# Optimization experiments

Measured on AMD Instinct MI355X. Metric: run time of the kernel, lower is better.

Reference implementation:

```python
import jax, jax.numpy as jnp
import numpy as np

B, A, N, D_IN, HID, H = 128, 64, 2000, 128, 512, 8
HD = HID // H  # head_dim = 64
ND = 16        # depot agents


def setup_inputs() -> dict:
    key = jax.random.key(0)
    ks = jax.random.split(key, 8)
    s = 0.05  # keep logits well-conditioned
    return {
        "state_t": jax.random.normal(ks[0], (B, A, D_IN), dtype=jnp.float32),
        "context": jax.random.normal(ks[1], (B, N, D_IN), dtype=jnp.float32),
        "context_d": jax.random.normal(ks[2], (B, N, D_IN), dtype=jnp.float32),
        "w_q": jax.random.normal(ks[3], (HID, D_IN), dtype=jnp.float32) * s,
        "w_k1": jax.random.normal(ks[4], (HID, D_IN), dtype=jnp.float32) * s,
        "w_v1": jax.random.normal(ks[5], (HID, D_IN), dtype=jnp.float32) * s,
        "w_fc": jax.random.normal(ks[6], (HID, HID), dtype=jnp.float32) * s,
        "w_k2": jax.random.normal(ks[7], (HID, D_IN), dtype=jnp.float32) * s,
        "n_d": ND,
        "mask": jax.random.randint(jax.random.fold_in(key, 1), (B, A, N), 0, 2, dtype=jnp.int32),
        "T": 1,
    }


def reference(state_t, context, context_d, w_q, w_k1, w_v1, w_fc, w_k2, n_d, mask, T):
    hidden = w_q.shape[0]
    hd = hidden // H
    norm1 = np.float32(1.0 / np.sqrt(hd))
    norm2 = np.float32(1.0 / np.sqrt(hidden))

    def attn1(st, ctx, m):
        b, a, _ = st.shape
        n = ctx.shape[1]
        Q = (st @ w_q.T).reshape(b, a, H, hd).transpose(0, 2, 1, 3)   # (b,H,a,hd)
        K = (ctx @ w_k1.T).reshape(b, n, H, hd).transpose(0, 2, 1, 3)  # (b,H,n,hd)
        V = (ctx @ w_v1.T).reshape(b, n, H, hd).transpose(0, 2, 1, 3)
        comp = norm1 * jnp.einsum('bhad,bhnd->bhan', Q, K)
        u = jnp.where(m[:, None, :, :] != 0, jnp.float32(-10000.0), comp)
        s = jax.nn.softmax(u, axis=-1)
        out = jnp.einsum('bhan,bhnd->bhad', s, V)
        # FAITHFUL to torch: .view(b, a, hidden) on (b,H,a,hd) WITHOUT head transpose
        return out.reshape(b, a, hidden) @ w_fc.T

    x_d = attn1(state_t[:, :n_d], context_d, mask[:, :n_d])       # (B, n_d, HID)
    x_r = attn1(state_t[:, n_d:], context, mask[:, n_d:])         # (B, A-n_d, HID)

    Kd = context_d @ w_k2.T  # (B, N, HID)
    Kr = context @ w_k2.T
    compd = norm2 * jnp.einsum('bad,bnd->ban', x_d, Kd)
    compr = norm2 * jnp.einsum('bad,bnd->ban', x_r, Kr)
    comp = jnp.concatenate([compd, compr], axis=1)                # (B, A, N)
    comp = jnp.where(mask != 0, jnp.float32(-10000.0), comp)
    return jax.nn.softmax(comp / T, axis=-1)
```

## Files before the change

### kernel.cpp

```cpp
#include <hip/hip_runtime.h>

typedef short s16x8 __attribute__((ext_vector_type(8)));
typedef float f32x4 __attribute__((ext_vector_type(4)));

#define B_   128
#define A_   64
#define N_   2000
#define DIN  128
#define HID  512
#define H_   8
#define HD_  64
#define ND_  16
#define NT_  32

__device__ __forceinline__ unsigned short f2bf(float f) {
  union { float f; unsigned int u; } v; v.f = f;
  unsigned int u = v.u;
  unsigned int r = (u + 0x7fffu + ((u >> 16) & 1u)) >> 16;
  return (unsigned short)r;
}

__device__ __forceinline__ float bf2f(unsigned int u16v) {
  union { unsigned int u; float f; } v; v.u = u16v << 16;
  return v.f;
}

__device__ __forceinline__ f32x4 mfma16(s16x8 a, s16x8 b, f32x4 c) {
  return __builtin_amdgcn_mfma_f32_16x16x32_bf16(a, b, c, 0, 0, 0);
}

__device__ __forceinline__ unsigned int cvtpk(float lo, float hi) {
  unsigned int r;
  asm("v_cvt_pk_bf16_f32 %0, %1, %2" : "=v"(r) : "v"(lo), "v"(hi));
  return r;
}

__device__ __forceinline__ void gload16(const void* g, void* l) {
  __builtin_amdgcn_global_load_lds(
      (const __attribute__((address_space(1))) unsigned int*)g,
      (__attribute__((address_space(3))) unsigned int*)l, 16, 0, 0);
}

__device__ __forceinline__ void barrier_lds() {
  asm volatile("s_waitcnt lgkmcnt(0)" ::: "memory");
  __builtin_amdgcn_s_barrier();
  __builtin_amdgcn_sched_barrier(0);
}
__device__ __forceinline__ void barrier_full() {
  asm volatile("s_waitcnt vmcnt(0) lgkmcnt(0)" ::: "memory");
  __builtin_amdgcn_s_barrier();
  __builtin_amdgcn_sched_barrier(0);
}

__global__ __launch_bounds__(256) void k_cvt(const float* __restrict__ src,
                                             unsigned short* __restrict__ dst, int n4) {
  int i = blockIdx.x * blockDim.x + threadIdx.x;
  int stride = gridDim.x * blockDim.x;
  for (; i < n4; i += stride) {
    float4 v = ((const float4*)src)[i];
    ushort4 o;
    o.x = f2bf(v.x); o.y = f2bf(v.y); o.z = f2bf(v.z); o.w = f2bf(v.w);
    ((ushort4*)dst)[i] = o;
  }
}

__global__ __launch_bounds__(256) void k_cvt_t(const float* __restrict__ src,
                                               unsigned short* __restrict__ dst) {
  int i = blockIdx.x * 256 + threadIdx.x;
  int o = i >> 7, d = i & 127;
  dst[d * 512 + o] = f2bf(src[i]);
}

__global__ __launch_bounds__(256) void k_mask(const int* __restrict__ src,
                                              unsigned char* __restrict__ dst, int n4) {
  int i = blockIdx.x * blockDim.x + threadIdx.x;
  int stride = gridDim.x * blockDim.x;
  for (; i < n4; i += stride) {
    int4 v = ((const int4*)src)[i];
    uchar4 o;
    o.x = v.x ? 1 : 0; o.y = v.y ? 1 : 0; o.z = v.z ? 1 : 0; o.w = v.w ? 1 : 0;
    ((uchar4*)dst)[i] = o;
  }
}

template <int BR>
__device__ __forceinline__ void attn_body(
    int sub,
    const unsigned short* __restrict__ st, const unsigned short* __restrict__ C,
    const unsigned short* __restrict__ wq, const unsigned short* __restrict__ wk1,
    const unsigned short* __restrict__ wv1, const unsigned char* __restrict__ mask,
    float* __restrict__ x,
    unsigned short (*ctx_lds)[128], unsigned short (*K_lds)[72],
    unsigned short (*VT_lds)[72], unsigned short (*QP_lds)[72], float (*red_l)[48]) {
  constexpr int AT = BR ? 3 : 1;
  constexpr int a0 = BR ? ND_ : 0;
  const int tid = threadIdx.x;
  const int w = tid >> 6, lane = tid & 63, rn = lane & 15, kq = lane >> 4;
  const int b = sub >> 3, h = sub & 7;
  const int srow = lane >> 4;
  const int scol = lane & 15;

#pragma unroll
  for (int i = 0; i < 4; ++i) {
    int r0 = i * 16 + w * 4;
    int row = r0 + srow;
    const char* g = (const char*)C + (((size_t)b * N_ + row) << 8) + ((scol ^ (row & 7)) << 4);
    gload16(g, (char*)&ctx_lds[0][0] + (r0 << 8));
  }

  s16x8 kfrag[4], vfrag[4];
  {
    const size_t orow = (size_t)(h * HD_ + w * 16 + rn) * DIN;
#pragma unroll
    for (int k = 0; k < 4; ++k) {
      kfrag[k] = *(const s16x8*)(wk1 + orow + k * 32 + kq * 8);
      vfrag[k] = *(const s16x8*)(wv1 + orow + k * 32 + kq * 8);
    }
  }

  {
    s16x8 qw[4];
    const size_t orow = (size_t)(h * HD_ + w * 16 + rn) * DIN;
#pragma unroll
    for (int k = 0; k < 4; ++k) qw[k] = *(const s16x8*)(wq + orow + k * 32 + kq * 8);
#pragma unroll
    for (int at = 0; at < AT; ++at) {
      f32x4 acc = {0.f, 0.f, 0.f, 0.f};
#pragma unroll
      for (int k = 0; k < 4; ++k) {
        s16x8 sf = *(const s16x8*)(st + (size_t)(b * A_ + a0 + at * 16 + rn) * DIN + k * 32 + kq * 8);
        acc = mfma16(qw[k], sf, acc);
      }
      uint2 pk; pk.x = cvtpk(acc[0], acc[1]); pk.y = cvtpk(acc[2], acc[3]);
      *(uint2*)&QP_lds[at * 16 + rn][w * 16 + kq * 4] = pk;
    }
  }
  barrier_lds();

  s16x8 qf[AT][2];
#pragma unroll
  for (int at = 0; at < AT; ++at)
#pragma unroll
    for (int kd = 0; kd < 2; ++kd)
      qf[at][kd] = *(const s16x8*)&QP_lds[at * 16 + rn][kd * 32 + kq * 8];

  f32x4 O[AT];
  float lpart[AT];
#pragma unroll
  for (int at = 0; at < AT; ++at) { O[at] = {0.f, 0.f, 0.f, 0.f}; lpart[at] = 0.f; }

  for (int nt = 0; nt < NT_; ++nt) {
    const int n0 = nt * 64;
    barrier_full();

    unsigned int m4[AT];
    const int ngbase = n0 + w * 16 + kq * 4;
    const int ngc = ngbase > (N_ - 4) ? (N_ - 4) : ngbase;
#pragma unroll
    for (int at = 0; at < AT; ++at)
      m4[at] = *(const unsigned int*)(mask + (size_t)(b * A_ + a0 + at * 16 + rn) * N_ + ngc);

#pragma unroll
    for (int ns = 0; ns < 4; ++ns) {
      s16x8 cf[4];
#pragma unroll
      for (int kd = 0; kd < 4; ++kd)
        cf[kd] = *(const s16x8*)&ctx_lds[ns * 16 + rn][(((kd << 2) | kq) ^ (rn & 7)) << 3];
      f32x4 aK = {0.f, 0.f, 0.f, 0.f}, aV = {0.f, 0.f, 0.f, 0.f};
#pragma unroll
      for (int kd = 0; kd < 4; ++kd) {
        aK = mfma16(kfrag[kd], cf[kd], aK);
        aV = mfma16(cf[kd], vfrag[kd], aV);
      }
      if (n0 + 64 > N_) {
#pragma unroll
        for (int r = 0; r < 4; ++r)
          if (n0 + ns * 16 + kq * 4 + r >= N_) aV[r] = 0.f;
      }
      uint2 pkK; pkK.x = cvtpk(aK[0], aK[1]); pkK.y = cvtpk(aK[2], aK[3]);
      *(uint2*)&K_lds[ns * 16 + rn][w * 16 + kq * 4] = pkK;
      uint2 pkV; pkV.x = cvtpk(aV[0], aV[1]); pkV.y = cvtpk(aV[2], aV[3]);
      *(uint2*)&VT_lds[w * 16 + rn][ns * 16 + kq * 4] = pkV;
    }
    barrier_lds();

    if (nt + 1 < NT_) {
      const int n1 = n0 + 64;
#pragma unroll
      for (int i = 0; i < 4; ++i) {
        int r0 = i * 16 + w * 4;
        int row = r0 + srow;
        const char* g = (const char*)C + (((size_t)b * N_ + n1 + row) << 8) + ((scol ^ (row & 7)) << 4);
        gload16(g, (char*)&ctx_lds[0][0] + (r0 << 8));
      }
    }

    s16x8 kf[2];
#pragma unroll
    for (int kd = 0; kd < 2; ++kd)
      kf[kd] = *(const s16x8*)&K_lds[w * 16 + rn][kd * 32 + kq * 8];
#pragma unroll
    for (int at = 0; at < AT; ++at) {
      f32x4 acc = {0.f, 0.f, 0.f, 0.f};
#pragma unroll
      for (int kd = 0; kd < 2; ++kd) acc = mfma16(kf[kd], qf[at][kd], acc);
      float p[4];
#pragma unroll
      for (int r = 0; r < 4; ++r) {
        bool valid = (ngbase + r < N_) && (((m4[at] >> (8 * r)) & 255u) == 0u);
        float e = valid ? acc[r] * 0.125f - 8.0f : -1.0e4f;
        p[r] = __expf(e);
      }
      lpart[at] += (p[0] + p[1]) + (p[2] + p[3]);
      uint2 pkP; pkP.x = cvtpk(p[0], p[1]); pkP.y = cvtpk(p[2], p[3]);
      *(uint2*)&QP_lds[at * 16 + rn][w * 16 + kq * 4] = pkP;
    }
    barrier_lds();

    s16x8 vtf[2];
#pragma unroll
    for (int kn = 0; kn < 2; ++kn)
      vtf[kn] = *(const s16x8*)&VT_lds[w * 16 + rn][kn * 32 + kq * 8];
#pragma unroll
    for (int at = 0; at < AT; ++at) {
      f32x4 acc = O[at];
#pragma unroll
      for (int kn = 0; kn < 2; ++kn)
        acc = mfma16(*(const s16x8*)&QP_lds[at * 16 + rn][kn * 32 + kq * 8], vtf[kn], acc);
      O[at] = acc;
    }
  }

#pragma unroll
  for (int at = 0; at < AT; ++at) {
    float lp = lpart[at];
    lp += __shfl_xor(lp, 16);
    lp += __shfl_xor(lp, 32);
    if (kq == 0) red_l[w][at * 16 + rn] = lp;
  }
  barrier_lds();
#pragma unroll
  for (int at = 0; at < AT; ++at) {
#pragma unroll
    for (int r = 0; r < 4; ++r) {
      int a = at * 16 + kq * 4 + r;
      float ls = (red_l[0][a] + red_l[1][a]) + (red_l[2][a] + red_l[3][a]);
      float val = O[at][r] / ls;
      int row = BR ? (ND_ + h * 6 + (a >> 3)) : (h * 2 + (a >> 3));
      int col = (a & 7) * HD_ + w * 16 + rn;
      x[((size_t)b * A_ + row) * HID + col] = val;
    }
  }
}

__global__ __launch_bounds__(256) void k_attn1(const unsigned short* __restrict__ st,
                                               const unsigned short* __restrict__ ctx,
                                               const unsigned short* __restrict__ ctxd,
                                               const unsigned short* __restrict__ wq,
                                               const unsigned short* __restrict__ wk1,
                                               const unsigned short* __restrict__ wv1,
                                               const unsigned char* __restrict__ mask,
                                               float* __restrict__ x) {
  __shared__ unsigned short ctx_lds[64][128];
  __shared__ unsigned short K_lds[64][72];
  __shared__ unsigned short VT_lds[64][72];
  __shared__ unsigned short QP_lds[48][72];
  __shared__ float red_l[4][48];
  const int bid = blockIdx.x;
  const int sub = bid >> 1;
  if (bid & 1)
    attn_body<1>(sub, st, ctx, wq, wk1, wv1, mask, x, ctx_lds, K_lds, VT_lds, QP_lds, red_l);
  else
    attn_body<0>(sub, st, ctxd, wq, wk1, wv1, mask, x, ctx_lds, K_lds, VT_lds, QP_lds, red_l);
}

__global__ __launch_bounds__(256) void k_fc2(const float* __restrict__ x,
                                             const unsigned short* __restrict__ wfc,
                                             const unsigned short* __restrict__ wk2t,
                                             unsigned short* __restrict__ y2b) {
  __shared__ unsigned short x2_lds[16][520];
  const int tid = threadIdx.x;
  const int w = tid >> 6;
  const int lane = tid & 63;
  const int rn = lane & 15, kq = lane >> 4;
  const size_t rowbase = (size_t)blockIdx.x * 16;
  const float norm2 = 0.04419417382415922f;

  f32x4 acc[8];
#pragma unroll
  for (int ot = 0; ot < 8; ++ot) acc[ot] = {0.f, 0.f, 0.f, 0.f};

  for (int k = 0; k < 16; ++k) {
    const float* ap = x + (rowbase + rn) * HID + k * 32 + kq * 8;
    float4 a1 = *(const float4*)ap;
    float4 a2 = *(const float4*)(ap + 4);
    s16x8 af;
    af[0] = (short)f2bf(a1.x); af[1] = (short)f2bf(a1.y);
    af[2] = (short)f2bf(a1.z); af[3] = (short)f2bf(a1.w);
    af[4] = (short)f2bf(a2.x); af[5] = (short)f2bf(a2.y);
    af[6] = (short)f2bf(a2.z); af[7] = (short)f2bf(a2.w);
#pragma unroll
    for (int ot = 0; ot < 8; ++ot) {
      s16x8 bf = *(const s16x8*)(wfc + (size_t)(w * 128 + ot * 16 + rn) * HID + k * 32 + kq * 8);
      acc[ot] = mfma16(af, bf, acc[ot]);
    }
  }
#pragma unroll
  for (int ot = 0; ot < 8; ++ot)
#pragma unroll
    for (int r = 0; r < 4; ++r)
      x2_lds[kq * 4 + r][w * 128 + ot * 16 + rn] = f2bf(acc[ot][r]);
  __syncthreads();

#pragma unroll
  for (int j = 0; j < 2; ++j) {
    const int d0 = w * 32 + j * 16;
    f32x4 acc2 = {0.f, 0.f, 0.f, 0.f};
    for (int kk = 0; kk < 16; ++kk) {
      s16x8 af2 = *(const s16x8*)&x2_lds[rn][kk * 32 + kq * 8];
      s16x8 bf2 = *(const s16x8*)(wk2t + (size_t)(d0 + rn) * HID + kk * 32 + kq * 8);
      acc2 = mfma16(af2, bf2, acc2);
    }
#pragma unroll
    for (int r = 0; r < 4; ++r)
      y2b[(rowbase + kq * 4 + r) * DIN + d0 + rn] = f2bf(acc2[r] * norm2);
  }
}

__global__ __launch_bounds__(256) void k_logits_sm(const unsigned short* __restrict__ ctx,
                                                   const unsigned short* __restrict__ ctxd,
                                                   const unsigned short* __restrict__ y2b,
                                                   const unsigned char* __restrict__ mask,
                                                   const int* __restrict__ Tptr,
                                                   float* __restrict__ out) {
  __shared__ unsigned short ctx_lds[3][64][128];
  __shared__ unsigned short p_lds[16][2048];
  __shared__ float red_l[4][16];

  const int tid = threadIdx.x;
  const int w = tid >> 6, lane = tid & 63, rn = lane & 15, kq = lane >> 4;
  const int atile = blockIdx.x;
  const int b = blockIdx.y;
  const int a0 = atile * 16;
  const unsigned short* __restrict__ C = atile ? ctx : ctxd;
  const float Tinv = 1.0f / (float)Tptr[0];
  const int srow = lane >> 4, scol = lane & 15;
  const size_t bN = (size_t)b * N_;
  const size_t mrow = (size_t)(b * A_ + a0 + rn) * N_;

  s16x8 yf[4];
#pragma unroll
  for (int kd = 0; kd < 4; ++kd)
    yf[kd] = *(const s16x8*)(y2b + (size_t)(b * A_ + a0 + rn) * DIN + kd * 32 + kq * 8);

  unsigned int mcur = *(const unsigned int*)(mask + mrow + w * 16 + kq * 4);
#pragma unroll
  for (int i = 0; i < 4; ++i) {
    int r0 = i * 16 + w * 4;
    int row = r0 + srow;
    gload16((const char*)C + ((bN + row) << 8) + ((scol ^ (row & 7)) << 4),
            (char*)&ctx_lds[0][0][0] + (r0 << 8));
  }
#pragma unroll
  for (int i = 0; i < 4; ++i) {
    int r0 = i * 16 + w * 4;
    int row = r0 + srow;
    gload16((const char*)C + ((bN + 64 + row) << 8) + ((scol ^ (row & 7)) << 4),
            (char*)&ctx_lds[1][0][0] + (r0 << 8));
  }

  float lpart = 0.f;
  for (int nt = 0; nt < NT_; ++nt) {
    const int n0 = nt * 64;
    if (nt == 0) { asm volatile("s_waitcnt vmcnt(4)" ::: "memory"); }
    else         { asm volatile("s_waitcnt vmcnt(5)" ::: "memory"); }
    __builtin_amdgcn_s_barrier();
    __builtin_amdgcn_sched_barrier(0);

    unsigned int mnext;
    {
      int nb1 = (nt + 1 < NT_ ? nt + 1 : 0) * 64 + w * 16 + kq * 4;
      int ngc = nb1 > (N_ - 4) ? (N_ - 4) : nb1;
      mnext = *(const unsigned int*)(mask + mrow + ngc);
    }
    {
      int t2 = nt + 2 < NT_ ? nt + 2 : 0;
      char* dstb = (char*)&ctx_lds[(nt + 2) % 3][0][0];
#pragma unroll
      for (int i = 0; i < 4; ++i) {
        int r0 = i * 16 + w * 4;
        int row = r0 + srow;
        gload16((const char*)C + ((bN + t2 * 64 + row) << 8) + ((scol ^ (row & 7)) << 4),
                dstb + (r0 << 8));
      }
    }

    const unsigned short (*buf)[128] = ctx_lds[nt % 3];
    f32x4 acc = {0.f, 0.f, 0.f, 0.f};
#pragma unroll
    for (int kd = 0; kd < 4; ++kd) {
      s16x8 cf = *(const s16x8*)&buf[w * 16 + rn][(((kd << 2) | kq) ^ (rn & 7)) << 3];
      acc = mfma16(cf, yf[kd], acc);
    }
    const int nbase = n0 + w * 16 + kq * 4;
    float pv[4];
#pragma unroll
    for (int r = 0; r < 4; ++r) {
      bool valid = (nbase + r < N_) && (((mcur >> (8 * r)) & 255u) == 0u);
      pv[r] = valid ? __expf(acc[r] * Tinv - 8.0f) : 0.f;
    }
    lpart += (pv[0] + pv[1]) + (pv[2] + pv[3]);
    uint2 pk; pk.x = cvtpk(pv[0], pv[1]); pk.y = cvtpk(pv[2], pv[3]);
    int bo = (rn << 12) + (nbase << 1);
    *(uint2*)((char*)p_lds + (bo ^ ((rn & 7) << 4))) = pk;
    mcur = mnext;
  }

  float lp = lpart;
  lp += __shfl_xor(lp, 16);
  lp += __shfl_xor(lp, 32);
  if (kq == 0) red_l[w][rn] = lp;
  barrier_full();

  const size_t outbase = ((size_t)b * A_ + a0) * (size_t)N_;
  for (int row = 0; row < 16; ++row) {
    float l = (red_l[0][row] + red_l[1][row]) + (red_l[2][row] + red_l[3][row]);
    float inv = 1.0f / l;
    if (tid < 250) {
      const char* srcp = (const char*)p_lds + (row << 12) + ((tid ^ (row & 7)) << 4);
      uint2 pk = *(const uint2*)srcp;
      float4 o0, o1;
      o0.x = bf2f(pk.x & 0xFFFFu) * inv;
      o0.y = bf2f(pk.x >> 16) * inv;
      o0.z = bf2f(pk.y & 0xFFFFu) * inv;
      o0.w = bf2f(pk.y >> 16) * inv;
      const char* srcp2 = srcp + 8;
      uint2 pk2 = *(const uint2*)srcp2;
      o1.x = bf2f(pk2.x & 0xFFFFu) * inv;
      o1.y = bf2f(pk2.x >> 16) * inv;
      o1.z = bf2f(pk2.y & 0xFFFFu) * inv;
      o1.w = bf2f(pk2.y >> 16) * inv;
      float* op = out + outbase + (size_t)row * N_ + tid * 8;
      *(float4*)op = o0;
      *(float4*)(op + 4) = o1;
    }
  }
}

extern "C" void kernel_launch(void* const* d_in, const int* in_sizes, int n_in,
                              void* d_out, int out_size, void* d_ws, size_t ws_size,
                              hipStream_t stream) {
  const float* state_t   = (const float*)d_in[0];
  const float* context   = (const float*)d_in[1];
  const float* context_d = (const float*)d_in[2];
  const float* w_q  = (const float*)d_in[3];
  const float* w_k1 = (const float*)d_in[4];
  const float* w_v1 = (const float*)d_in[5];
  const float* w_fc = (const float*)d_in[6];
  const float* w_k2 = (const float*)d_in[7];
  const int* maski  = (const int*)d_in[9];
  const int* Tptr   = (const int*)d_in[10];
  float* out = (float*)d_out;

  char* ws = (char*)d_ws;
  unsigned short* ctxb  = (unsigned short*)ws; ws += (size_t)B_ * N_ * DIN * 2;
  unsigned short* ctxdb = (unsigned short*)ws; ws += (size_t)B_ * N_ * DIN * 2;
  unsigned short* stb   = (unsigned short*)ws; ws += (size_t)B_ * A_ * DIN * 2;
  unsigned short* wqb   = (unsigned short*)ws; ws += (size_t)HID * DIN * 2;
  unsigned short* wk1b  = (unsigned short*)ws; ws += (size_t)HID * DIN * 2;
  unsigned short* wv1b  = (unsigned short*)ws; ws += (size_t)HID * DIN * 2;
  unsigned short* wk2t  = (unsigned short*)ws; ws += (size_t)HID * DIN * 2;
  unsigned short* wfcb  = (unsigned short*)ws; ws += (size_t)HID * HID * 2;
  unsigned char*  mask8 = (unsigned char*)ws;  ws += (size_t)B_ * A_ * N_;
  float*          x     = (float*)ws;          ws += (size_t)B_ * A_ * HID * 4;
  unsigned short* y2b   = (unsigned short*)ws; ws += (size_t)B_ * A_ * DIN * 2;

  k_cvt<<<2048, 256, 0, stream>>>(context,   ctxb,  B_ * N_ * DIN / 4);
  k_cvt<<<2048, 256, 0, stream>>>(context_d, ctxdb, B_ * N_ * DIN / 4);
  k_cvt<<<256,  256, 0, stream>>>(state_t,   stb,   B_ * A_ * DIN / 4);
  k_cvt<<<64,   256, 0, stream>>>(w_q,  wqb,  HID * DIN / 4);
  k_cvt<<<64,   256, 0, stream>>>(w_k1, wk1b, HID * DIN / 4);
  k_cvt<<<64,   256, 0, stream>>>(w_v1, wv1b, HID * DIN / 4);
  k_cvt_t<<<256, 256, 0, stream>>>(w_k2, wk2t);
  k_cvt<<<256,  256, 0, stream>>>(w_fc, wfcb, HID * HID / 4);
  k_mask<<<2048, 256, 0, stream>>>(maski, mask8, B_ * A_ * N_ / 4);

  k_attn1<<<2048, 256, 0, stream>>>(stb, ctxb, ctxdb, wqb, wk1b, wv1b, mask8, x);

  k_fc2<<<(B_ * A_) / 16, 256, 0, stream>>>(x, wfcb, wk2t, y2b);

  dim3 gl(4, B_);
  k_logits_sm<<<gl, 256, 0, stream>>>(ctxb, ctxdb, y2b, mask8, Tptr, out);
}
```

Before: 486.5 us.

## Restructure attention kernel per-wave N tiles, double-buffer context, drop mask conversion

```diff
diff --git a/kernel.cpp b/kernel.cpp
--- a/kernel.cpp
+++ b/kernel.cpp
@@ -31,7 +31,7 @@
 
 __device__ __forceinline__ unsigned int cvtpk(float lo, float hi) {
   unsigned int r;
-  asm("v_cvt_pk_bf16_f32 %0, %1, %2" : "=v"(r) : "v"(lo), "v"(hi));
+  asm("v_cvt_pk_bf16_f32 %0, %1, %2" : "=&v"(r) : "v"(lo), "v"(hi));
   return r;
 }
 
@@ -41,11 +41,6 @@
       (__attribute__((address_space(3))) unsigned int*)l, 16, 0, 0);
 }
 
-__device__ __forceinline__ void barrier_lds() {
-  asm volatile("s_waitcnt lgkmcnt(0)" ::: "memory");
-  __builtin_amdgcn_s_barrier();
-  __builtin_amdgcn_sched_barrier(0);
-}
 __device__ __forceinline__ void barrier_full() {
   asm volatile("s_waitcnt vmcnt(0) lgkmcnt(0)" ::: "memory");
   __builtin_amdgcn_s_barrier();
@@ -71,184 +66,208 @@
   dst[d * 512 + o] = f2bf(src[i]);
 }
 
-__global__ __launch_bounds__(256) void k_mask(const int* __restrict__ src,
-                                              unsigned char* __restrict__ dst, int n4) {
-  int i = blockIdx.x * blockDim.x + threadIdx.x;
-  int stride = gridDim.x * blockDim.x;
-  for (; i < n4; i += stride) {
-    int4 v = ((const int4*)src)[i];
-    uchar4 o;
-    o.x = v.x ? 1 : 0; o.y = v.y ? 1 : 0; o.z = v.z ? 1 : 0; o.w = v.w ? 1 : 0;
-    ((uchar4*)dst)[i] = o;
-  }
-}
-
 template <int BR>
 __device__ __forceinline__ void attn_body(
     int sub,
     const unsigned short* __restrict__ st, const unsigned short* __restrict__ C,
     const unsigned short* __restrict__ wq, const unsigned short* __restrict__ wk1,
-    const unsigned short* __restrict__ wv1, const unsigned char* __restrict__ mask,
-    float* __restrict__ x,
-    unsigned short (*ctx_lds)[128], unsigned short (*K_lds)[72],
-    unsigned short (*VT_lds)[72], unsigned short (*QP_lds)[72], float (*red_l)[48]) {
+    const unsigned short* __restrict__ wv1, const int* __restrict__ maski,
+    float* __restrict__ x, char* smem) {
   constexpr int AT = BR ? 3 : 1;
   constexpr int a0 = BR ? ND_ : 0;
   const int tid = threadIdx.x;
   const int w = tid >> 6, lane = tid & 63, rn = lane & 15, kq = lane >> 4;
   const int b = sub >> 3, h = sub & 7;
-  const int srow = lane >> 4;
-  const int scol = lane & 15;
+
+  unsigned short (*K_w)[72]  = (unsigned short (*)[72])(smem + 32768 + w * 2304);
+  unsigned short (*VT_w)[40] = (unsigned short (*)[40])(smem + 41984 + w * 5120);
+  unsigned short (*Q_lds)[72] = (unsigned short (*)[72])(smem + 62464);
+  unsigned short (*P_w)[40]  = (unsigned short (*)[40])(smem + 62464 + w * 3840);
 
 #pragma unroll
   for (int i = 0; i < 4; ++i) {
-    int r0 = i * 16 + w * 4;
-    int row = r0 + srow;
-    const char* g = (const char*)C + (((size_t)b * N_ + row) << 8) + ((scol ^ (row & 7)) << 4);
-    gload16(g, (char*)&ctx_lds[0][0] + (r0 << 8));
-  }
-
-  s16x8 kfrag[4], vfrag[4];
-  {
-    const size_t orow = (size_t)(h * HD_ + w * 16 + rn) * DIN;
-#pragma unroll
-    for (int k = 0; k < 4; ++k) {
-      kfrag[k] = *(const s16x8*)(wk1 + orow + k * 32 + kq * 8);
-      vfrag[k] = *(const s16x8*)(wv1 + orow + k * 32 + kq * 8);
-    }
+    int r0 = i * 16 + w * 4, row = r0 + kq;
+    gload16((const char*)C + (((size_t)b * N_ + row) << 8) + ((rn ^ (row & 7)) << 4),
+            smem + (r0 << 8));
   }
 
   {
     s16x8 qw[4];
-    const size_t orow = (size_t)(h * HD_ + w * 16 + rn) * DIN;
-#pragma unroll
-    for (int k = 0; k < 4; ++k) qw[k] = *(const s16x8*)(wq + orow + k * 32 + kq * 8);
+#pragma unroll
+    for (int kd = 0; kd < 4; ++kd)
+      qw[kd] = *(const s16x8*)(wq + (size_t)(h * HD_ + w * 16 + rn) * DIN + kd * 32 + kq * 8);
 #pragma unroll
     for (int at = 0; at < AT; ++at) {
       f32x4 acc = {0.f, 0.f, 0.f, 0.f};
 #pragma unroll
-      for (int k = 0; k < 4; ++k) {
-        s16x8 sf = *(const s16x8*)(st + (size_t)(b * A_ + a0 + at * 16 + rn) * DIN + k * 32 + kq * 8);
-        acc = mfma16(qw[k], sf, acc);
+      for (int kd = 0; kd < 4; ++kd) {
+        s16x8 sf = *(const s16x8*)(st + (size_t)(b * A_ + a0 + at * 16 + rn) * DIN + kd * 32 + kq * 8);
+        acc = mfma16(qw[kd], sf, acc);
       }
       uint2 pk; pk.x = cvtpk(acc[0], acc[1]); pk.y = cvtpk(acc[2], acc[3]);
-      *(uint2*)&QP_lds[at * 16 + rn][w * 16 + kq * 4] = pk;
-    }
-  }
-  barrier_lds();
+      *(uint2*)&Q_lds[at * 16 + rn][w * 16 + kq * 4] = pk;
+    }
+  }
+
+  s16x8 kfrag[4][4], vfrag[4][4];
+#pragma unroll
+  for (int s = 0; s < 4; ++s) {
+    const size_t orow = (size_t)(h * HD_ + s * 16 + rn) * DIN;
+#pragma unroll
+    for (int kd = 0; kd < 4; ++kd) {
+      kfrag[s][kd] = *(const s16x8*)(wk1 + orow + kd * 32 + kq * 8);
+      vfrag[s][kd] = *(const s16x8*)(wv1 + orow + kd * 32 + kq * 8);
+    }
+  }
+
+  __syncthreads();
 
   s16x8 qf[AT][2];
 #pragma unroll
   for (int at = 0; at < AT; ++at)
 #pragma unroll
     for (int kd = 0; kd < 2; ++kd)
-      qf[at][kd] = *(const s16x8*)&QP_lds[at * 16 + rn][kd * 32 + kq * 8];
-
-  f32x4 O[AT];
+      qf[at][kd] = *(const s16x8*)&Q_lds[at * 16 + rn][kd * 32 + kq * 8];
+
+  __syncthreads();
+
+  {
+    uint2 z; z.x = 0u; z.y = 0u;
+#pragma unroll
+    for (int at = 0; at < AT; ++at)
+      *(uint2*)&P_w[at * 16 + rn][kq * 8 + 4] = z;
+#pragma unroll
+    for (int s = 0; s < 4; ++s)
+      *(uint2*)&VT_w[s * 16 + rn][kq * 8 + 4] = z;
+  }
+
+  f32x4 O[AT][4];
   float lpart[AT];
 #pragma unroll
-  for (int at = 0; at < AT; ++at) { O[at] = {0.f, 0.f, 0.f, 0.f}; lpart[at] = 0.f; }
+  for (int at = 0; at < AT; ++at) {
+    lpart[at] = 0.f;
+#pragma unroll
+    for (int s = 0; s < 4; ++s) O[at][s] = {0.f, 0.f, 0.f, 0.f};
+  }
+
+  const size_t mbase = (size_t)(b * A_ + a0 + rn) * N_;
 
   for (int nt = 0; nt < NT_; ++nt) {
+    __syncthreads();
     const int n0 = nt * 64;
-    barrier_full();
-
-    unsigned int m4[AT];
-    const int ngbase = n0 + w * 16 + kq * 4;
-    const int ngc = ngbase > (N_ - 4) ? (N_ - 4) : ngbase;
+
+    int4 mv[AT];
+    const int ngb = n0 + w * 16 + kq * 4;
+    const int ngc = ngb > (N_ - 4) ? (N_ - 4) : ngb;
 #pragma unroll
     for (int at = 0; at < AT; ++at)
-      m4[at] = *(const unsigned int*)(mask + (size_t)(b * A_ + a0 + at * 16 + rn) * N_ + ngc);
-
-#pragma unroll
-    for (int ns = 0; ns < 4; ++ns) {
-      s16x8 cf[4];
-#pragma unroll
-      for (int kd = 0; kd < 4; ++kd)
-        cf[kd] = *(const s16x8*)&ctx_lds[ns * 16 + rn][(((kd << 2) | kq) ^ (rn & 7)) << 3];
-      f32x4 aK = {0.f, 0.f, 0.f, 0.f}, aV = {0.f, 0.f, 0.f, 0.f};
-#pragma unroll
-      for (int kd = 0; kd < 4; ++kd) {
-        aK = mfma16(kfrag[kd], cf[kd], aK);
-        aV = mfma16(cf[kd], vfrag[kd], aV);
+      mv[at] = *(const int4*)(maski + mbase + (size_t)(at * 16) * N_ + ngc);
+
+    if (nt + 1 < NT_) {
+      char* dst = smem + ((nt + 1) & 1) * 16384;
+#pragma unroll
+      for (int i = 0; i < 4; ++i) {
+        int r0 = i * 16 + w * 4, row = r0 + kq;
+        int rg = n0 + 64 + row; rg = rg < N_ ? rg : (N_ - 1);
+        gload16((const char*)C + (((size_t)b * N_ + rg) << 8) + ((rn ^ (row & 7)) << 4),
+                dst + (r0 << 8));
       }
-      if (n0 + 64 > N_) {
-#pragma unroll
-        for (int r = 0; r < 4; ++r)
-          if (n0 + ns * 16 + kq * 4 + r >= N_) aV[r] = 0.f;
-      }
-      uint2 pkK; pkK.x = cvtpk(aK[0], aK[1]); pkK.y = cvtpk(aK[2], aK[3]);
-      *(uint2*)&K_lds[ns * 16 + rn][w * 16 + kq * 4] = pkK;
-      uint2 pkV; pkV.x = cvtpk(aV[0], aV[1]); pkV.y = cvtpk(aV[2], aV[3]);
-      *(uint2*)&VT_lds[w * 16 + rn][ns * 16 + kq * 4] = pkV;
-    }
-    barrier_lds();
-
-    if (nt + 1 < NT_) {
-      const int n1 = n0 + 64;
-#pragma unroll
-      for (int i = 0; i < 4; ++i) {
-        int r0 = i * 16 + w * 4;
-        int row = r0 + srow;
-        const char* g = (const char*)C + (((size_t)b * N_ + n1 + row) << 8) + ((scol ^ (row & 7)) << 4);
-        gload16(g, (char*)&ctx_lds[0][0] + (r0 << 8));
-      }
+    }
+
+    const unsigned short (*buf)[128] = (const unsigned short (*)[128])(smem + (nt & 1) * 16384);
+    s16x8 cf[4];
+#pragma unroll
+    for (int kd = 0; kd < 4; ++kd)
+      cf[kd] = *(const s16x8*)&buf[w * 16 + rn][(((kd << 2) | kq) ^ (rn & 7)) << 3];
+
+#pragma unroll
+    for (int s = 0; s < 4; ++s) {
+      f32x4 aK = {0.f, 0.f, 0.f, 0.f};
+#pragma unroll
+      for (int kd = 0; kd < 4; ++kd) aK = mfma16(kfrag[s][kd], cf[kd], aK);
+      uint2 pk; pk.x = cvtpk(aK[0], aK[1]); pk.y = cvtpk(aK[2], aK[3]);
+      *(uint2*)&K_w[rn][s * 16 + kq * 4] = pk;
+    }
+
+#pragma unroll
+    for (int s = 0; s < 4; ++s) {
+      f32x4 aV = {0.f, 0.f, 0.f, 0.f};
+#pragma unroll
+      for (int kd = 0; kd < 4; ++kd) aV = mfma16(cf[kd], vfrag[s][kd], aV);
+      uint2 pk; pk.x = cvtpk(aV[0], aV[1]); pk.y = cvtpk(aV[2], aV[3]);
+      *(uint2*)&VT_w[s * 16 + rn][kq * 8] = pk;
     }
 
     s16x8 kf[2];
 #pragma unroll
     for (int kd = 0; kd < 2; ++kd)
-      kf[kd] = *(const s16x8*)&K_lds[w * 16 + rn][kd * 32 + kq * 8];
+      kf[kd] = *(const s16x8*)&K_w[rn][kd * 32 + kq * 8];
 #pragma unroll
     for (int at = 0; at < AT; ++at) {
       f32x4 acc = {0.f, 0.f, 0.f, 0.f};
-#pragma unroll
-      for (int kd = 0; kd < 2; ++kd) acc = mfma16(kf[kd], qf[at][kd], acc);
-      float p[4];
-#pragma unroll
-      for (int r = 0; r < 4; ++r) {
-        bool valid = (ngbase + r < N_) && (((m4[at] >> (8 * r)) & 255u) == 0u);
-        float e = valid ? acc[r] * 0.125f - 8.0f : -1.0e4f;
-        p[r] = __expf(e);
-      }
-      lpart[at] += (p[0] + p[1]) + (p[2] + p[3]);
-      uint2 pkP; pkP.x = cvtpk(p[0], p[1]); pkP.y = cvtpk(p[2], p[3]);
-      *(uint2*)&QP_lds[at * 16 + rn][w * 16 + kq * 4] = pkP;
-    }
-    barrier_lds();
-
-    s16x8 vtf[2];
-#pragma unroll
-    for (int kn = 0; kn < 2; ++kn)
-      vtf[kn] = *(const s16x8*)&VT_lds[w * 16 + rn][kn * 32 + kq * 8];
+      acc = mfma16(kf[0], qf[at][0], acc);
+      acc = mfma16(kf[1], qf[at][1], acc);
+      float p0 = ((ngb + 0 < N_) && (mv[at].x == 0)) ? __expf(acc[0] * 0.125f - 8.0f) : 0.f;
+      float p1 = ((ngb + 1 < N_) && (mv[at].y == 0)) ? __expf(acc[1] * 0.125f - 8.0f) : 0.f;
+      float p2 = ((ngb + 2 < N_) && (mv[at].z == 0)) ? __expf(acc[2] * 0.125f - 8.0f) : 0.f;
+      float p3 = ((ngb + 3 < N_) && (mv[at].w == 0)) ? __expf(acc[3] * 0.125f - 8.0f) : 0.f;
+      lpart[at] += (p0 + p1) + (p2 + p3);
+      uint2 pk; pk.x = cvtpk(p0, p1); pk.y = cvtpk(p2, p3);
+      *(uint2*)&P_w[at * 16 + rn][kq * 8] = pk;
+    }
+
+    s16x8 vtf[4];
+#pragma unroll
+    for (int s = 0; s < 4; ++s)
+      vtf[s] = *(const s16x8*)&VT_w[s * 16 + rn][kq * 8];
 #pragma unroll
     for (int at = 0; at < AT; ++at) {
-      f32x4 acc = O[at];
-#pragma unroll
-      for (int kn = 0; kn < 2; ++kn)
-        acc = mfma16(*(const s16x8*)&QP_lds[at * 16 + rn][kn * 32 + kq * 8], vtf[kn], acc);
-      O[at] = acc;
-    }
-  }
-
+      s16x8 pa = *(const s16x8*)&P_w[at * 16 + rn][kq * 8];
+#pragma unroll
+      for (int s = 0; s < 4; ++s)
+        O[at][s] = mfma16(pa, vtf[s], O[at][s]);
+    }
+  }
+
+  __syncthreads();
+  float* redl = (float*)smem;
+  float* lsum = (float*)(smem + 1024);
+  float* redO = (float*)(smem + 2048);
 #pragma unroll
   for (int at = 0; at < AT; ++at) {
     float lp = lpart[at];
     lp += __shfl_xor(lp, 16);
     lp += __shfl_xor(lp, 32);
-    if (kq == 0) red_l[w][at * 16 + rn] = lp;
-  }
-  barrier_lds();
-#pragma unroll
-  for (int at = 0; at < AT; ++at) {
-#pragma unroll
-    for (int r = 0; r < 4; ++r) {
-      int a = at * 16 + kq * 4 + r;
-      float ls = (red_l[0][a] + red_l[1][a]) + (red_l[2][a] + red_l[3][a]);
-      float val = O[at][r] / ls;
-      int row = BR ? (ND_ + h * 6 + (a >> 3)) : (h * 2 + (a >> 3));
-      int col = (a & 7) * HD_ + w * 16 + rn;
-      x[((size_t)b * A_ + row) * HID + col] = val;
+    if (kq == 0) redl[w * 48 + at * 16 + rn] = lp;
+  }
+  __syncthreads();
+  if (tid < 16 * AT) lsum[tid] = redl[tid] + redl[48 + tid] + redl[96 + tid] + redl[144 + tid];
+
+#pragma unroll
+  for (int p = 0; p < 2; ++p) {
+    __syncthreads();
+#pragma unroll
+    for (int at = 0; at < AT; ++at)
+#pragma unroll
+      for (int q = 0; q < 2; ++q)
+        *(f32x4*)&redO[(w * 6 + at * 2 + q) * 256 + lane * 4] = O[at][p * 2 + q];
+    __syncthreads();
+    for (int t = w; t < 2 * AT; t += 4) {
+      int at = t >> 1;
+      int sp = p * 2 + (t & 1);
+      f32x4 v  = *(const f32x4*)&redO[(0 * 6 + t) * 256 + lane * 4];
+      f32x4 v1 = *(const f32x4*)&redO[(1 * 6 + t) * 256 + lane * 4];
+      f32x4 v2 = *(const f32x4*)&redO[(2 * 6 + t) * 256 + lane * 4];
+      f32x4 v3 = *(const f32x4*)&redO[(3 * 6 + t) * 256 + lane * 4];
+      v = (v + v1) + (v2 + v3);
+#pragma unroll
+      for (int r = 0; r < 4; ++r) {
+        int a_idx = at * 16 + kq * 4 + r;
+        float ls = lsum[at * 16 + kq * 4 + r];
+        int d = sp * 16 + rn;
+        int row = BR ? (ND_ + h * 6 + (a_idx >> 3)) : (h * 2 + (a_idx >> 3));
+        x[((size_t)b * A_ + row) * HID + (a_idx & 7) * HD_ + d] = v[r] / ls;
+      }
     }
   }
 }
@@ -259,19 +278,15 @@
                                                const unsigned short* __restrict__ wq,
                                                const unsigned short* __restrict__ wk1,
                                                const unsigned short* __restrict__ wv1,
-                                               const unsigned char* __restrict__ mask,
+                                               const int* __restrict__ maski,
                                                float* __restrict__ x) {
-  __shared__ unsigned short ctx_lds[64][128];
-  __shared__ unsigned short K_lds[64][72];
-  __shared__ unsigned short VT_lds[64][72];
-  __shared__ unsigned short QP_lds[48][72];
-  __shared__ float red_l[4][48];
+  __shared__ __align__(16) char smem[77824];
   const int bid = blockIdx.x;
   const int sub = bid >> 1;
   if (bid & 1)
-    attn_body<1>(sub, st, ctx, wq, wk1, wv1, mask, x, ctx_lds, K_lds, VT_lds, QP_lds, red_l);
+    attn_body<1>(sub, st, ctx, wq, wk1, wv1, maski, x, smem);
   else
-    attn_body<0>(sub, st, ctxd, wq, wk1, wv1, mask, x, ctx_lds, K_lds, VT_lds, QP_lds, red_l);
+    attn_body<0>(sub, st, ctxd, wq, wk1, wv1, maski, x, smem);
 }
 
 __global__ __launch_bounds__(256) void k_fc2(const float* __restrict__ x,
@@ -330,7 +345,7 @@
 __global__ __launch_bounds__(256) void k_logits_sm(const unsigned short* __restrict__ ctx,
                                                    const unsigned short* __restrict__ ctxd,
                                                    const unsigned short* __restrict__ y2b,
-                                                   const unsigned char* __restrict__ mask,
+                                                   const int* __restrict__ maski,
                                                    const int* __restrict__ Tptr,
                                                    float* __restrict__ out) {
   __shared__ unsigned short ctx_lds[3][64][128];
@@ -353,7 +368,7 @@
   for (int kd = 0; kd < 4; ++kd)
     yf[kd] = *(const s16x8*)(y2b + (size_t)(b * A_ + a0 + rn) * DIN + kd * 32 + kq * 8);
 
-  unsigned int mcur = *(const unsigned int*)(mask + mrow + w * 16 + kq * 4);
+  int4 mcur = *(const int4*)(maski + mrow + w * 16 + kq * 4);
 #pragma unroll
   for (int i = 0; i < 4; ++i) {
     int r0 = i * 16 + w * 4;
@@ -377,11 +392,11 @@
     __builtin_amdgcn_s_barrier();
     __builtin_amdgcn_sched_barrier(0);
 
-    unsigned int mnext;
+    int4 mnext;
     {
       int nb1 = (nt + 1 < NT_ ? nt + 1 : 0) * 64 + w * 16 + kq * 4;
       int ngc = nb1 > (N_ - 4) ? (N_ - 4) : nb1;
-      mnext = *(const unsigned int*)(mask + mrow + ngc);
+      mnext = *(const int4*)(maski + mrow + ngc);
     }
     {
       int t2 = nt + 2 < NT_ ? nt + 2 : 0;
@@ -403,14 +418,12 @@
       acc = mfma16(cf, yf[kd], acc);
     }
     const int nbase = n0 + w * 16 + kq * 4;
-    float pv[4];
-#pragma unroll
-    for (int r = 0; r < 4; ++r) {
-      bool valid = (nbase + r < N_) && (((mcur >> (8 * r)) & 255u) == 0u);
-      pv[r] = valid ? __expf(acc[r] * Tinv - 8.0f) : 0.f;
-    }
-    lpart += (pv[0] + pv[1]) + (pv[2] + pv[3]);
-    uint2 pk; pk.x = cvtpk(pv[0], pv[1]); pk.y = cvtpk(pv[2], pv[3]);
+    float pv0 = ((nbase + 0 < N_) && (mcur.x == 0)) ? __expf(acc[0] * Tinv - 8.0f) : 0.f;
+    float pv1 = ((nbase + 1 < N_) && (mcur.y == 0)) ? __expf(acc[1] * Tinv - 8.0f) : 0.f;
+    float pv2 = ((nbase + 2 < N_) && (mcur.z == 0)) ? __expf(acc[2] * Tinv - 8.0f) : 0.f;
+    float pv3 = ((nbase + 3 < N_) && (mcur.w == 0)) ? __expf(acc[3] * Tinv - 8.0f) : 0.f;
+    lpart += (pv0 + pv1) + (pv2 + pv3);
+    uint2 pk; pk.x = cvtpk(pv0, pv1); pk.y = cvtpk(pv2, pv3);
     int bo = (rn << 12) + (nbase << 1);
     *(uint2*)((char*)p_lds + (bo ^ ((rn & 7) << 4))) = pk;
     mcur = mnext;
@@ -434,8 +447,7 @@
       o0.y = bf2f(pk.x >> 16) * inv;
       o0.z = bf2f(pk.y & 0xFFFFu) * inv;
       o0.w = bf2f(pk.y >> 16) * inv;
-      const char* srcp2 = srcp + 8;
-      uint2 pk2 = *(const uint2*)srcp2;
+      uint2 pk2 = *(const uint2*)(srcp + 8);
       o1.x = bf2f(pk2.x & 0xFFFFu) * inv;
       o1.y = bf2f(pk2.x >> 16) * inv;
       o1.z = bf2f(pk2.y & 0xFFFFu) * inv;
@@ -471,7 +483,6 @@
   unsigned short* wv1b  = (unsigned short*)ws; ws += (size_t)HID * DIN * 2;
   unsigned short* wk2t  = (unsigned short*)ws; ws += (size_t)HID * DIN * 2;
   unsigned short* wfcb  = (unsigned short*)ws; ws += (size_t)HID * HID * 2;
-  unsigned char*  mask8 = (unsigned char*)ws;  ws += (size_t)B_ * A_ * N_;
   float*          x     = (float*)ws;          ws += (size_t)B_ * A_ * HID * 4;
   unsigned short* y2b   = (unsigned short*)ws; ws += (size_t)B_ * A_ * DIN * 2;
 
@@ -483,12 +494,11 @@
   k_cvt<<<64,   256, 0, stream>>>(w_v1, wv1b, HID * DIN / 4);
   k_cvt_t<<<256, 256, 0, stream>>>(w_k2, wk2t);
   k_cvt<<<256,  256, 0, stream>>>(w_fc, wfcb, HID * HID / 4);
-  k_mask<<<2048, 256, 0, stream>>>(maski, mask8, B_ * A_ * N_ / 4);
-
-  k_attn1<<<2048, 256, 0, stream>>>(stb, ctxb, ctxdb, wqb, wk1b, wv1b, mask8, x);
+
+  k_attn1<<<2048, 256, 0, stream>>>(stb, ctxb, ctxdb, wqb, wk1b, wv1b, maski, x);
 
   k_fc2<<<(B_ * A_) / 16, 256, 0, stream>>>(x, wfcb, wk2t, y2b);
 
   dim3 gl(4, B_);
-  k_logits_sm<<<gl, 256, 0, stream>>>(ctxb, ctxdb, y2b, mask8, Tptr, out);
-}
+  k_logits_sm<<<gl, 256, 0, stream>>>(ctxb, ctxdb, y2b, maski, Tptr, out);
+}
```

Measured after the change: 651.4 us. +33.9%, slower.
